# Kernel tuning notes

Hardware: AMD Instinct MI355X
Metric: run time of the kernel (lower is better)

Reference implementation:

```python
import jax, jax.numpy as jnp
import numpy as np

IN_F = 4096
OUT_F = 4096
N_VALS = 4096
N_TOKENS = 4096


def setup_inputs() -> dict:
    key = jax.random.key(0)
    k_x, k_v, k_i = jax.random.split(key, 3)
    x = jax.random.normal(k_x, (N_TOKENS, IN_F), dtype=jnp.float32)
    # codebook of memristor conductance differences (sorted, as in load_values)
    values = jnp.sort(jax.random.normal(k_v, (N_VALS,), dtype=jnp.float32))
    w_idx = jax.random.randint(k_i, (OUT_F, IN_F), 0, N_VALS, dtype=jnp.int64)
    bias = jnp.zeros((OUT_F,), dtype=jnp.float32)
    return {"x": x, "values": values, "w_idx": w_idx, "bias": bias}


def reference(x, values, w_idx, bias):
    # dequantize weight from codebook: (out_f, in_f)
    weight = values[w_idx]
    # F.linear(x, weight, bias) == x @ weight.T + bias
    return jnp.einsum("ti,oi->to", x, weight) + bias
```

## Files before the change

kernel.cpp:

```cpp
#include <hip/hip_runtime.h>
#include <hip/hip_bf16.h>
#include <stdint.h>

typedef unsigned short u16;
typedef __bf16 bf16x8 __attribute__((ext_vector_type(8)));
typedef float  f32x4  __attribute__((ext_vector_type(4)));
typedef u16    u16x8  __attribute__((ext_vector_type(8)));
typedef u16    u16x4  __attribute__((ext_vector_type(4)));

__device__ __forceinline__ u16 f2bf(float f) {
  union { float f; unsigned u; } v; v.f = f;
  unsigned u = v.u;
  unsigned r = u + 0x7FFFu + ((u >> 16) & 1u);
  return (u16)(r >> 16);
}

__device__ __forceinline__ void gld_lds16(const void* g, void* l) {
  __builtin_amdgcn_global_load_lds(
      (const __attribute__((address_space(1))) void*)g,
      (__attribute__((address_space(3))) void*)l, 16, 0, 0);
}

__global__ void detect_idx_width(const unsigned* __restrict__ w, int* __restrict__ flag) {
  unsigned v = w[threadIdx.x * 2 + 1];
  unsigned long long any = __ballot(v != 0u);
  if (threadIdx.x == 0) *flag = (any != 0ull) ? 1 : 0;
}

__global__ __launch_bounds__(256) void cvt_x_kernel(const float4* __restrict__ x,
                                                    u16* __restrict__ xb, long n8) {
  long i = (long)blockIdx.x * blockDim.x + threadIdx.x;
  long stride = (long)gridDim.x * blockDim.x;
  for (; i < n8; i += stride) {
    float4 a = x[2 * i];
    float4 b = x[2 * i + 1];
    u16x8 r;
    r[0] = f2bf(a.x); r[1] = f2bf(a.y); r[2] = f2bf(a.z); r[3] = f2bf(a.w);
    r[4] = f2bf(b.x); r[5] = f2bf(b.y); r[6] = f2bf(b.z); r[7] = f2bf(b.w);
    *(u16x8*)(xb + 8 * i) = r;
  }
}

__global__ __launch_bounds__(256) void dequant_w_kernel(const int4* __restrict__ widx,
                                                        const float* __restrict__ values,
                                                        u16* __restrict__ wb,
                                                        const int* __restrict__ flag, long n4) {
  const bool is32 = (*flag != 0);
  long i = (long)blockIdx.x * blockDim.x + threadIdx.x;
  long stride = (long)gridDim.x * blockDim.x;
  for (; i < n4; i += stride) {
    int i0, i1, i2, i3;
    if (is32) {
      int4 v = widx[i];
      i0 = v.x; i1 = v.y; i2 = v.z; i3 = v.w;
    } else {
      int4 a = widx[2 * i];
      int4 b = widx[2 * i + 1];
      i0 = a.x; i1 = a.z; i2 = b.x; i3 = b.z;
    }
    u16x4 r;
    r[0] = f2bf(values[i0]); r[1] = f2bf(values[i1]);
    r[2] = f2bf(values[i2]); r[3] = f2bf(values[i3]);
    *(u16x4*)(wb + 4 * i) = r;
  }
}

#define VMW(n) asm volatile("s_waitcnt vmcnt(" #n ")" ::: "memory")
#define PH_BAR asm volatile("s_barrier" ::: "memory")

__global__ __launch_bounds__(512, 1) void gemm256_kernel(
    const u16* __restrict__ Xb, const u16* __restrict__ Wb,
    const float* __restrict__ bias, float* __restrict__ C,
    int Nout, int Kin) {
  __shared__ __align__(16) char lds[163840];

  const int tid  = threadIdx.x;
  const int lane = tid & 63;
  const int wave = tid >> 6;
  const int wr = wave >> 2;
  const int wc = wave & 3;

  const int nwg = gridDim.x;
  const int bid = blockIdx.x;
  const int q8 = nwg >> 3, r8 = nwg & 7;
  const int xcd = bid & 7;
  const int wg = (xcd < r8 ? xcd * (q8 + 1) : r8 * (q8 + 1) + (xcd - r8) * q8) + (bid >> 3);

  const int tiles_n = Nout / 256;
  const long brow = (long)(wg / tiles_n) * 256;
  const long bcol = (long)(wg % tiles_n) * 256;

  const long rowb = (long)Kin * 2;
  const long rstep = 64 * rowb;
  const long hstep = 128 * rowb;

  const int f0  = tid * 16;
  const int f1  = f0 + 8192;
  const int rS0 = f0 >> 7;
  const int cS  = (f0 & 127) ^ ((rS0 & 7) << 4);
  const int voff = (int)(rS0 * rowb) + cS;

  const char* uA = (const char*)Xb + (size_t)brow * rowb;
  const char* uB = (const char*)Wb + (size_t)bcol * rowb;

#define STAGE_AH(base_, h, t) { \
  gld_lds16(uA + (size_t)(h) * hstep + (size_t)(t) * 128 + voff,         lds + (base_) + (h) * 16384 + f0); \
  gld_lds16(uA + (size_t)(h) * hstep + (size_t)(t) * 128 + rstep + voff, lds + (base_) + (h) * 16384 + f1); }
#define STAGE_BH(base_, h, t) { \
  gld_lds16(uB + (size_t)(h) * hstep + (size_t)(t) * 128 + voff,         lds + (base_) + (h) * 16384 + f0); \
  gld_lds16(uB + (size_t)(h) * hstep + (size_t)(t) * 128 + rstep + voff, lds + (base_) + (h) * 16384 + f1); }

  const int fr   = lane & 15;
  const int kb   = (lane >> 4) * 16;
  const int xsw  = (fr & 7) << 4;
  const int colx0 = kb ^ xsw;
  const int colx1 = (64 + kb) ^ xsw;
  const int aOff = wr * 16384 + fr * 128;
  const int bOff = (wc >> 1) * 16384 + ((wc & 1) * 64 + fr) * 128;

  bf16x8 afrA[2][2];
  bf16x8 afrB[2][2];
  bf16x8 bfrE[4][2];
  bf16x8 bfrO[4][2];
  f32x4  acc[8][4] = {};

#define READ_AQ(abase_, q, DST) { \
  const char* ab = lds + (abase_) + aOff + (q) * 4096; \
  DST[0][0] = *(const bf16x8*)(ab + colx0); \
  DST[0][1] = *(const bf16x8*)(ab + colx1); \
  DST[1][0] = *(const bf16x8*)(ab + 2048 + colx0); \
  DST[1][1] = *(const bf16x8*)(ab + 2048 + colx1); }

#define READ_BPF(bbase_, dst, lo) { \
  const char* bb = lds + (bbase_) + bOff; \
  dst[(lo)][0]     = *(const bf16x8*)(bb + (lo) * 2048 + colx0); \
  dst[(lo)][1]     = *(const bf16x8*)(bb + (lo) * 2048 + colx1); \
  dst[(lo) + 1][0] = *(const bf16x8*)(bb + ((lo) + 1) * 2048 + colx0); \
  dst[(lo) + 1][1] = *(const bf16x8*)(bb + ((lo) + 1) * 2048 + colx1); }

#define MFMA_Q(q, AF, BF) { \
  __builtin_amdgcn_s_setprio(1); \
  _Pragma("unroll") for (int m2 = 0; m2 < 2; ++m2) \
  _Pragma("unroll") for (int ni = 0; ni < 4; ++ni) { \
    acc[(q)*2+m2][ni] = __builtin_amdgcn_mfma_f32_16x16x32_bf16(AF[m2][0], BF[ni][0], acc[(q)*2+m2][ni], 0, 0, 0); \
    acc[(q)*2+m2][ni] = __builtin_amdgcn_mfma_f32_16x16x32_bf16(AF[m2][1], BF[ni][1], acc[(q)*2+m2][ni], 0, 0, 0); } \
  __builtin_amdgcn_s_setprio(0); }

#define PHASE(RDS, STG, MF, WT) { \
  RDS; STG; PH_BAR; MF; WT; PH_BAR; }

  const int aB0 = 0, aB1 = 32768;
  int bR0 = 65536, bR1 = 98304, bR2 = 131072;
  const int NT = Kin >> 6;

  STAGE_AH(aB0, 0, 0); STAGE_AH(aB0, 1, 0);
  STAGE_BH(bR0, 0, 0); STAGE_BH(bR0, 1, 0);
  if (NT > 1) { STAGE_BH(bR1, 0, 1); STAGE_BH(bR1, 1, 1); }
  if (NT > 2) { STAGE_BH(bR2, 0, 2); STAGE_BH(bR2, 1, 2); }
  VMW(0);
  PH_BAR;
  READ_BPF(bR0, bfrE, 0); READ_BPF(bR0, bfrE, 2);

  const int NITER = NT >> 1;
  for (int i = 0; i < NITER; ++i) {
    const int t0 = i * 2;
    const bool a1 = (t0 + 1 < NT);
    const bool a2 = (t0 + 2 < NT);
    const bool b3 = (t0 + 3 < NT);
    const bool b4 = (t0 + 4 < NT);

    PHASE({ READ_AQ(aB0, 0, afrA); READ_AQ(aB0, 1, afrB); },
          { if (a1) STAGE_AH(aB1, 0, t0 + 1); },
          MFMA_Q(0, afrA, bfrE), (void)0);
    PHASE({ READ_AQ(aB0, 2, afrA); if (a1) READ_BPF(bR1, bfrO, 0); },
          { if (a1) STAGE_AH(aB1, 1, t0 + 1); },
          MFMA_Q(1, afrB, bfrE), (void)0);
    PHASE({ READ_AQ(aB0, 3, afrB); if (a1) READ_BPF(bR1, bfrO, 2); },
          { if (b3) STAGE_BH(bR0, 0, t0 + 3); },
          MFMA_Q(2, afrA, bfrE), (void)0);
    PHASE({ (void)0; },
          { if (b3) STAGE_BH(bR0, 1, t0 + 3); },
          MFMA_Q(3, afrB, bfrE),
          { if (b3) { VMW(4); } else { VMW(0); } });

    PHASE({ READ_AQ(aB1, 0, afrA); READ_AQ(aB1, 1, afrB); },
          { if (a2) STAGE_AH(aB0, 0, t0 + 2); },
          MFMA_Q(0, afrA, bfrO), (void)0);
    PHASE({ READ_AQ(aB1, 2, afrA); if (a2) READ_BPF(bR2, bfrE, 0); },
          { if (a2) STAGE_AH(aB0, 1, t0 + 2); },
          MFMA_Q(1, afrB, bfrO), (void)0);
    PHASE({ READ_AQ(aB1, 3, afrB); if (a2) READ_BPF(bR2, bfrE, 2); },
          { if (b4) STAGE_BH(bR1, 0, t0 + 4); },
          MFMA_Q(2, afrA, bfrO), (void)0);
    PHASE({ (void)0; },
          { if (b4) STAGE_BH(bR1, 1, t0 + 4); },
          MFMA_Q(3, afrB, bfrO),
          { if (b4) { VMW(4); } else { VMW(0); } });

    int tmp = bR0; bR0 = bR2; bR2 = bR1; bR1 = tmp;
  }

  const int cm = (lane >> 4) * 4;
  const int cn = lane & 15;
  float bv[4];
#pragma unroll
  for (int ni = 0; ni < 4; ++ni) bv[ni] = bias[bcol + wc * 64 + ni * 16 + cn];

#pragma unroll
  for (int mi = 0; mi < 8; ++mi) {
    const long row0 = brow + wr * 128 + mi * 16 + cm;
#pragma unroll
    for (int ni = 0; ni < 4; ++ni) {
      const long col = bcol + wc * 64 + ni * 16 + cn;
#pragma unroll
      for (int j = 0; j < 4; ++j)
        C[(row0 + j) * (long)Nout + col] = acc[mi][ni][j] + bv[ni];
    }
  }
#undef STAGE_AH
#undef STAGE_BH
#undef READ_AQ
#undef READ_BPF
#undef MFMA_Q
#undef PHASE
}

__global__ __launch_bounds__(256, 2) void gemm128_kernel(
    const u16* __restrict__ Xb, const u16* __restrict__ Wb,
    const float* __restrict__ bias, float* __restrict__ C,
    int Nout, int Kin) {
  __shared__ __align__(16) u16 As[128 * 32];
  __shared__ __align__(16) u16 Bs[128 * 32];
  const int tid  = threadIdx.x;
  const int lane = tid & 63;
  const int wave = tid >> 6;
  const int wr = wave >> 1, wc = wave & 1;
  const int nwg = gridDim.x, bid = blockIdx.x;
  const int q = nwg >> 3, r8 = nwg & 7;
  const int xcd = bid & 7;
  const int wg = (xcd < r8 ? xcd * (q + 1) : r8 * (q + 1) + (xcd - r8) * q) + (bid >> 3);
  const int tiles_n = Nout / 128;
  const long brow = (long)(wg / tiles_n) * 128;
  const long bcol = (long)(wg % tiles_n) * 128;
  const int f0 = tid * 16, f1 = f0 + 4096;
  const size_t rowbytes = (size_t)Kin * 2;
  const char* gA0 = (const char*)Xb + (size_t)(brow + (f0 >> 6)) * rowbytes + (f0 & 63);
  const char* gA1 = (const char*)Xb + (size_t)(brow + (f1 >> 6)) * rowbytes + (f1 & 63);
  const char* gB0 = (const char*)Wb + (size_t)(bcol + (f0 >> 6)) * rowbytes + (f0 & 63);
  const char* gB1 = (const char*)Wb + (size_t)(bcol + (f1 >> 6)) * rowbytes + (f1 & 63);
  char* lA0 = (char*)As + f0; char* lA1 = (char*)As + f1;
  char* lB0 = (char*)Bs + f0; char* lB1 = (char*)Bs + f1;
  const int fr = lane & 15, kb = (lane >> 4) * 16;
  const char* aptr[4]; const char* bptr[4];
#pragma unroll
  for (int i = 0; i < 4; ++i) {
    aptr[i] = (const char*)As + (wr * 64 + i * 16 + fr) * 64 + kb;
    bptr[i] = (const char*)Bs + (wc * 64 + i * 16 + fr) * 64 + kb;
  }
  f32x4 acc[4][4] = {};
  for (int kk = 0; kk < Kin; kk += 32) {
    const size_t ko = (size_t)kk * 2;
    gld_lds16(gA0 + ko, lA0); gld_lds16(gA1 + ko, lA1);
    gld_lds16(gB0 + ko, lB0); gld_lds16(gB1 + ko, lB1);
    __syncthreads();
    bf16x8 a[4], b[4];
#pragma unroll
    for (int i = 0; i < 4; ++i) a[i] = *(const bf16x8*)aptr[i];
#pragma unroll
    for (int i = 0; i < 4; ++i) b[i] = *(const bf16x8*)bptr[i];
#pragma unroll
    for (int mi = 0; mi < 4; ++mi)
#pragma unroll
      for (int ni = 0; ni < 4; ++ni)
        acc[mi][ni] = __builtin_amdgcn_mfma_f32_16x16x32_bf16(a[mi], b[ni], acc[mi][ni], 0, 0, 0);
    __syncthreads();
  }
  const int cm = (lane >> 4) * 4, cn = lane & 15;
  float bv[4];
#pragma unroll
  for (int ni = 0; ni < 4; ++ni) bv[ni] = bias[bcol + wc * 64 + ni * 16 + cn];
#pragma unroll
  for (int mi = 0; mi < 4; ++mi) {
    const long row0 = brow + wr * 64 + mi * 16 + cm;
#pragma unroll
    for (int ni = 0; ni < 4; ++ni) {
      const long col = bcol + wc * 64 + ni * 16 + cn;
#pragma unroll
      for (int j = 0; j < 4; ++j)
        C[(row0 + j) * (long)Nout + col] = acc[mi][ni][j] + bv[ni];
    }
  }
}

__global__ void fallback_kernel(const float* __restrict__ x, const float* __restrict__ values,
                                const int* __restrict__ widx, const float* __restrict__ bias,
                                float* __restrict__ out, const int* __restrict__ flag,
                                int NT, int IF, int OF) {
  const int o = blockIdx.x * blockDim.x + threadIdx.x;
  const int t = blockIdx.y;
  if (o >= OF || t >= NT) return;
  const bool is32 = (*flag != 0);
  const float* xr = x + (size_t)t * IF;
  float sum = 0.f;
  if (is32) {
    const int* w = widx + (size_t)o * IF;
    for (int k = 0; k < IF; ++k) sum += xr[k] * values[w[k]];
  } else {
    const long long* w = (const long long*)widx + (size_t)o * IF;
    for (int k = 0; k < IF; ++k) sum += xr[k] * values[(int)w[k]];
  }
  out[(size_t)t * OF + o] = sum + bias[o];
}

extern "C" void kernel_launch(void* const* d_in, const int* in_sizes, int n_in,
                              void* d_out, int out_size, void* d_ws, size_t ws_size,
                              hipStream_t stream) {
  const float* x      = (const float*)d_in[0];
  const float* values = (const float*)d_in[1];
  const int*   widx   = (const int*)d_in[2];
  const float* bias   = (const float*)d_in[3];
  float* out = (float*)d_out;

  const long xsz = in_sizes[0];
  const int  OF  = in_sizes[3];
  const long wsz = in_sizes[2];
  const int  IF  = (int)(wsz / OF);
  const int  NTOK = (int)(xsz / IF);

  u16* xb = (u16*)d_ws;
  u16* wb = xb + (size_t)NTOK * IF;
  int* flag = (int*)(wb + (size_t)OF * IF);
  const size_t need = ((size_t)NTOK * IF + (size_t)OF * IF) * sizeof(u16) + 64;

  const bool pre_ok = (ws_size >= need) && ((xsz % 8) == 0) && ((wsz % 4) == 0);
  const bool f256 = pre_ok && (IF % 128 == 0) && (IF >= 256) &&
                    (NTOK % 256 == 0) && (OF % 256 == 0);
  const bool f128 = pre_ok && (IF % 32 == 0) && (NTOK % 128 == 0) && (OF % 128 == 0);

  if (f256 || f128) {
    hipLaunchKernelGGL(detect_idx_width, dim3(1), dim3(64), 0, stream,
                       (const unsigned*)widx, flag);
    hipLaunchKernelGGL(cvt_x_kernel, dim3(2048), dim3(256), 0, stream,
                       (const float4*)x, xb, xsz / 8);
    hipLaunchKernelGGL(dequant_w_kernel, dim3(2048), dim3(256), 0, stream,
                       (const int4*)widx, values, wb, (const int*)flag, wsz / 4);
    if (f256) {
      const int grid = (NTOK / 256) * (OF / 256);
      hipLaunchKernelGGL(gemm256_kernel, dim3(grid), dim3(512), 0, stream,
                         xb, wb, bias, out, OF, IF);
    } else {
      const int grid = (NTOK / 128) * (OF / 128);
      hipLaunchKernelGGL(gemm128_kernel, dim3(grid), dim3(256), 0, stream,
                         xb, wb, bias, out, OF, IF);
    }
  } else {
    int* flag2 = (int*)d_ws;
    hipLaunchKernelGGL(detect_idx_width, dim3(1), dim3(64), 0, stream,
                       (const unsigned*)widx, flag2);
    hipLaunchKernelGGL(fallback_kernel, dim3((OF + 255) / 256, NTOK), dim3(256), 0, stream,
                       x, values, widx, bias, out, (const int*)flag2, NTOK, IF, OF);
  }
}
```

Before: 170.8 us.

## Interleave LDS reads and global loads with MFMAs via sched_group_barrier; fuse prepass kernels

Rewrites the gemm256 main loop so that each phase interleaves individual MFMA pairs with single LDS fragment reads and global-to-LDS loads, using sched_group_barrier to pin the order. It also drops one barrier per phase, prefetches the next A fragment a phase ahead, and peels the last two iterations so the steady-state loop has no bounds checks. The x conversion and weight dequant kernels are merged into one launch. The aim is to hide LDS and global latency under matrix math and save a launch. The trade-off is fewer barriers with tighter wait counts, which raises the risk of LDS races, plus more register pressure from prefetched fragments.

After: 154.6 us. 9.5% less time.

```diff
diff --git a/kernel.cpp b/kernel.cpp
--- a/kernel.cpp
+++ b/kernel.cpp
@@ -27,11 +27,13 @@
   if (threadIdx.x == 0) *flag = (any != 0ull) ? 1 : 0;
 }
 
-__global__ __launch_bounds__(256) void cvt_x_kernel(const float4* __restrict__ x,
-                                                    u16* __restrict__ xb, long n8) {
-  long i = (long)blockIdx.x * blockDim.x + threadIdx.x;
-  long stride = (long)gridDim.x * blockDim.x;
-  for (; i < n8; i += stride) {
+__global__ __launch_bounds__(256) void prepass_kernel(
+    const float4* __restrict__ x, u16* __restrict__ xb, long n8,
+    const int4* __restrict__ widx, const float* __restrict__ values,
+    u16* __restrict__ wb, const int* __restrict__ flag, long n4) {
+  const long gid = (long)blockIdx.x * blockDim.x + threadIdx.x;
+  const long stride = (long)gridDim.x * blockDim.x;
+  for (long i = gid; i < n8; i += stride) {
     float4 a = x[2 * i];
     float4 b = x[2 * i + 1];
     u16x8 r;
@@ -39,16 +41,8 @@
     r[4] = f2bf(b.x); r[5] = f2bf(b.y); r[6] = f2bf(b.z); r[7] = f2bf(b.w);
     *(u16x8*)(xb + 8 * i) = r;
   }
-}
-
-__global__ __launch_bounds__(256) void dequant_w_kernel(const int4* __restrict__ widx,
-                                                        const float* __restrict__ values,
-                                                        u16* __restrict__ wb,
-                                                        const int* __restrict__ flag, long n4) {
   const bool is32 = (*flag != 0);
-  long i = (long)blockIdx.x * blockDim.x + threadIdx.x;
-  long stride = (long)gridDim.x * blockDim.x;
-  for (; i < n4; i += stride) {
+  for (long i = gid; i < n4; i += stride) {
     int i0, i1, i2, i3;
     if (is32) {
       int4 v = widx[i];
@@ -67,6 +61,8 @@
 
 #define VMW(n) asm volatile("s_waitcnt vmcnt(" #n ")" ::: "memory")
 #define PH_BAR asm volatile("s_barrier" ::: "memory")
+#define SGB(m, n) __builtin_amdgcn_sched_group_barrier((m), (n), 0)
+#define NOWT (void)0
 
 __global__ __launch_bounds__(512, 1) void gemm256_kernel(
     const u16* __restrict__ Xb, const u16* __restrict__ Wb,
@@ -90,7 +86,7 @@
   const long brow = (long)(wg / tiles_n) * 256;
   const long bcol = (long)(wg % tiles_n) * 256;
 
-  const long rowb = (long)Kin * 2;
+  const long rowb  = (long)Kin * 2;
   const long rstep = 64 * rowb;
   const long hstep = 128 * rowb;
 
@@ -103,12 +99,12 @@
   const char* uA = (const char*)Xb + (size_t)brow * rowb;
   const char* uB = (const char*)Wb + (size_t)bcol * rowb;
 
-#define STAGE_AH(base_, h, t) { \
-  gld_lds16(uA + (size_t)(h) * hstep + (size_t)(t) * 128 + voff,         lds + (base_) + (h) * 16384 + f0); \
-  gld_lds16(uA + (size_t)(h) * hstep + (size_t)(t) * 128 + rstep + voff, lds + (base_) + (h) * 16384 + f1); }
-#define STAGE_BH(base_, h, t) { \
-  gld_lds16(uB + (size_t)(h) * hstep + (size_t)(t) * 128 + voff,         lds + (base_) + (h) * 16384 + f0); \
-  gld_lds16(uB + (size_t)(h) * hstep + (size_t)(t) * 128 + rstep + voff, lds + (base_) + (h) * 16384 + f1); }
+#define SA1(base_, h, t, part) \
+  gld_lds16(uA + (size_t)(h) * hstep + (size_t)(t) * 128 + ((part) ? rstep : 0) + voff, \
+            lds + (base_) + (h) * 16384 + ((part) ? f1 : f0));
+#define SB1(base_, h, t, part) \
+  gld_lds16(uB + (size_t)(h) * hstep + (size_t)(t) * 128 + ((part) ? rstep : 0) + voff, \
+            lds + (base_) + (h) * 16384 + ((part) ? f1 : f0));
 
   const int fr   = lane & 15;
   const int kb   = (lane >> 4) * 16;
@@ -124,79 +120,118 @@
   bf16x8 bfrO[4][2];
   f32x4  acc[8][4] = {};
 
-#define READ_AQ(abase_, q, DST) { \
-  const char* ab = lds + (abase_) + aOff + (q) * 4096; \
-  DST[0][0] = *(const bf16x8*)(ab + colx0); \
-  DST[0][1] = *(const bf16x8*)(ab + colx1); \
-  DST[1][0] = *(const bf16x8*)(ab + 2048 + colx0); \
-  DST[1][1] = *(const bf16x8*)(ab + 2048 + colx1); }
-
-#define READ_BPF(bbase_, dst, lo) { \
-  const char* bb = lds + (bbase_) + bOff; \
-  dst[(lo)][0]     = *(const bf16x8*)(bb + (lo) * 2048 + colx0); \
-  dst[(lo)][1]     = *(const bf16x8*)(bb + (lo) * 2048 + colx1); \
-  dst[(lo) + 1][0] = *(const bf16x8*)(bb + ((lo) + 1) * 2048 + colx0); \
-  dst[(lo) + 1][1] = *(const bf16x8*)(bb + ((lo) + 1) * 2048 + colx1); }
-
-#define MFMA_Q(q, AF, BF) { \
-  __builtin_amdgcn_s_setprio(1); \
-  _Pragma("unroll") for (int m2 = 0; m2 < 2; ++m2) \
-  _Pragma("unroll") for (int ni = 0; ni < 4; ++ni) { \
-    acc[(q)*2+m2][ni] = __builtin_amdgcn_mfma_f32_16x16x32_bf16(AF[m2][0], BF[ni][0], acc[(q)*2+m2][ni], 0, 0, 0); \
-    acc[(q)*2+m2][ni] = __builtin_amdgcn_mfma_f32_16x16x32_bf16(AF[m2][1], BF[ni][1], acc[(q)*2+m2][ni], 0, 0, 0); } \
-  __builtin_amdgcn_s_setprio(0); }
-
-#define PHASE(RDS, STG, MF, WT) { \
-  RDS; STG; PH_BAR; MF; WT; PH_BAR; }
+#define RDA(abase_, q, DST, m2, ks) \
+  DST[(m2)][(ks)] = *(const bf16x8*)(lds + (abase_) + aOff + (q) * 4096 + (m2) * 2048 + ((ks) ? colx1 : colx0));
+#define RDB(bbase_, DST, ni, ks) \
+  DST[(ni)][(ks)] = *(const bf16x8*)(lds + (bbase_) + bOff + (ni) * 2048 + ((ks) ? colx1 : colx0));
+
+#define MFMA1(d, a, b) d = __builtin_amdgcn_mfma_f32_16x16x32_bf16((a), (b), (d), 0, 0, 0)
+#define MM2(q, m2, ni, AF, BF) { \
+  MFMA1(acc[(q)*2+(m2)][(ni)], AF[(m2)][0], BF[(ni)][0]); \
+  MFMA1(acc[(q)*2+(m2)][(ni)], AF[(m2)][1], BF[(ni)][1]); }
+
+#define PHASE(q, AF, BF, R0, R1, R2, R3, R4, R5, S0, S1, WT) { \
+  MM2(q, 0, 0, AF, BF); SGB(0x8, 2); R0; SGB(0x100, 1); \
+  MM2(q, 1, 0, AF, BF); SGB(0x8, 2); R1; SGB(0x100, 1); \
+  MM2(q, 0, 1, AF, BF); SGB(0x8, 2); R2; SGB(0x100, 1); \
+  MM2(q, 1, 1, AF, BF); SGB(0x8, 2); R3; SGB(0x100, 1); \
+  MM2(q, 0, 2, AF, BF); SGB(0x8, 2); R4; SGB(0x100, 1); \
+  MM2(q, 1, 2, AF, BF); SGB(0x8, 2); R5; SGB(0x100, 1); \
+  MM2(q, 0, 3, AF, BF); SGB(0x8, 2); S0; SGB(0x70, 1); \
+  MM2(q, 1, 3, AF, BF); SGB(0x8, 2); S1; SGB(0x70, 1); \
+  WT; PH_BAR; }
 
   const int aB0 = 0, aB1 = 32768;
   int bR0 = 65536, bR1 = 98304, bR2 = 131072;
   const int NT = Kin >> 6;
 
-  STAGE_AH(aB0, 0, 0); STAGE_AH(aB0, 1, 0);
-  STAGE_BH(bR0, 0, 0); STAGE_BH(bR0, 1, 0);
-  if (NT > 1) { STAGE_BH(bR1, 0, 1); STAGE_BH(bR1, 1, 1); }
-  if (NT > 2) { STAGE_BH(bR2, 0, 2); STAGE_BH(bR2, 1, 2); }
+  SA1(aB0, 0, 0, 0); SA1(aB0, 0, 0, 1); SA1(aB0, 1, 0, 0); SA1(aB0, 1, 0, 1);
+  SB1(bR0, 0, 0, 0); SB1(bR0, 0, 0, 1); SB1(bR0, 1, 0, 0); SB1(bR0, 1, 0, 1);
+  SB1(bR1, 0, 1, 0); SB1(bR1, 0, 1, 1); SB1(bR1, 1, 1, 0); SB1(bR1, 1, 1, 1);
+  SB1(bR2, 0, 2, 0); SB1(bR2, 0, 2, 1); SB1(bR2, 1, 2, 0); SB1(bR2, 1, 2, 1);
   VMW(0);
   PH_BAR;
-  READ_BPF(bR0, bfrE, 0); READ_BPF(bR0, bfrE, 2);
+  RDB(bR0, bfrE, 0, 0); RDB(bR0, bfrE, 0, 1); RDB(bR0, bfrE, 1, 0); RDB(bR0, bfrE, 1, 1);
+  RDB(bR0, bfrE, 2, 0); RDB(bR0, bfrE, 2, 1); RDB(bR0, bfrE, 3, 0); RDB(bR0, bfrE, 3, 1);
+  RDA(aB0, 0, afrA, 0, 0); RDA(aB0, 0, afrA, 0, 1); RDA(aB0, 0, afrA, 1, 0); RDA(aB0, 0, afrA, 1, 1);
 
   const int NITER = NT >> 1;
-  for (int i = 0; i < NITER; ++i) {
+  const int MAIN = NITER - 2;
+  for (int i = 0; i < MAIN; ++i) {
+    const int t0 = i * 2;
+    PHASE(0, afrA, bfrE,
+          RDA(aB0, 1, afrB, 0, 0), RDA(aB0, 1, afrB, 0, 1), RDA(aB0, 1, afrB, 1, 0), RDA(aB0, 1, afrB, 1, 1),
+          RDB(bR1, bfrO, 0, 0), RDB(bR1, bfrO, 0, 1),
+          SA1(aB1, 0, t0 + 1, 0), SA1(aB1, 0, t0 + 1, 1), NOWT);
+    PHASE(1, afrB, bfrE,
+          RDA(aB0, 2, afrA, 0, 0), RDA(aB0, 2, afrA, 0, 1), RDA(aB0, 2, afrA, 1, 0), RDA(aB0, 2, afrA, 1, 1),
+          RDB(bR1, bfrO, 1, 0), RDB(bR1, bfrO, 1, 1),
+          SA1(aB1, 1, t0 + 1, 0), SA1(aB1, 1, t0 + 1, 1), NOWT);
+    PHASE(2, afrA, bfrE,
+          RDA(aB0, 3, afrB, 0, 0), RDA(aB0, 3, afrB, 0, 1), RDA(aB0, 3, afrB, 1, 0), RDA(aB0, 3, afrB, 1, 1),
+          RDB(bR1, bfrO, 2, 0), RDB(bR1, bfrO, 2, 1),
+          SB1(bR0, 0, t0 + 3, 0), SB1(bR0, 0, t0 + 3, 1), VMW(2));
+    PHASE(3, afrB, bfrE,
+          RDA(aB1, 0, afrA, 0, 0), RDA(aB1, 0, afrA, 0, 1), RDA(aB1, 0, afrA, 1, 0), RDA(aB1, 0, afrA, 1, 1),
+          RDB(bR1, bfrO, 3, 0), RDB(bR1, bfrO, 3, 1),
+          SB1(bR0, 1, t0 + 3, 0), SB1(bR0, 1, t0 + 3, 1), NOWT);
+    PHASE(0, afrA, bfrO,
+          RDA(aB1, 1, afrB, 0, 0), RDA(aB1, 1, afrB, 0, 1), RDA(aB1, 1, afrB, 1, 0), RDA(aB1, 1, afrB, 1, 1),
+          RDB(bR2, bfrE, 0, 0), RDB(bR2, bfrE, 0, 1),
+          SA1(aB0, 0, t0 + 2, 0), SA1(aB0, 0, t0 + 2, 1), NOWT);
+    PHASE(1, afrB, bfrO,
+          RDA(aB1, 2, afrA, 0, 0), RDA(aB1, 2, afrA, 0, 1), RDA(aB1, 2, afrA, 1, 0), RDA(aB1, 2, afrA, 1, 1),
+          RDB(bR2, bfrE, 1, 0), RDB(bR2, bfrE, 1, 1),
+          SA1(aB0, 1, t0 + 2, 0), SA1(aB0, 1, t0 + 2, 1), NOWT);
+    PHASE(2, afrA, bfrO,
+          RDA(aB1, 3, afrB, 0, 0), RDA(aB1, 3, afrB, 0, 1), RDA(aB1, 3, afrB, 1, 0), RDA(aB1, 3, afrB, 1, 1),
+          RDB(bR2, bfrE, 2, 0), RDB(bR2, bfrE, 2, 1),
+          SB1(bR1, 0, t0 + 4, 0), SB1(bR1, 0, t0 + 4, 1), VMW(2));
+    PHASE(3, afrB, bfrO,
+          RDA(aB0, 0, afrA, 0, 0), RDA(aB0, 0, afrA, 0, 1), RDA(aB0, 0, afrA, 1, 0), RDA(aB0, 0, afrA, 1, 1),
+          RDB(bR2, bfrE, 3, 0), RDB(bR2, bfrE, 3, 1),
+          SB1(bR1, 1, t0 + 4, 0), SB1(bR1, 1, t0 + 4, 1), NOWT);
+    int tmp = bR0; bR0 = bR2; bR2 = bR1; bR1 = tmp;
+  }
+
+  for (int i = (MAIN > 0 ? MAIN : 0); i < NITER; ++i) {
     const int t0 = i * 2;
     const bool a1 = (t0 + 1 < NT);
     const bool a2 = (t0 + 2 < NT);
     const bool b3 = (t0 + 3 < NT);
     const bool b4 = (t0 + 4 < NT);
-
-    PHASE({ READ_AQ(aB0, 0, afrA); READ_AQ(aB0, 1, afrB); },
-          { if (a1) STAGE_AH(aB1, 0, t0 + 1); },
-          MFMA_Q(0, afrA, bfrE), (void)0);
-    PHASE({ READ_AQ(aB0, 2, afrA); if (a1) READ_BPF(bR1, bfrO, 0); },
-          { if (a1) STAGE_AH(aB1, 1, t0 + 1); },
-          MFMA_Q(1, afrB, bfrE), (void)0);
-    PHASE({ READ_AQ(aB0, 3, afrB); if (a1) READ_BPF(bR1, bfrO, 2); },
-          { if (b3) STAGE_BH(bR0, 0, t0 + 3); },
-          MFMA_Q(2, afrA, bfrE), (void)0);
-    PHASE({ (void)0; },
-          { if (b3) STAGE_BH(bR0, 1, t0 + 3); },
-          MFMA_Q(3, afrB, bfrE),
-          { if (b3) { VMW(4); } else { VMW(0); } });
-
-    PHASE({ READ_AQ(aB1, 0, afrA); READ_AQ(aB1, 1, afrB); },
-          { if (a2) STAGE_AH(aB0, 0, t0 + 2); },
-          MFMA_Q(0, afrA, bfrO), (void)0);
-    PHASE({ READ_AQ(aB1, 2, afrA); if (a2) READ_BPF(bR2, bfrE, 0); },
-          { if (a2) STAGE_AH(aB0, 1, t0 + 2); },
-          MFMA_Q(1, afrB, bfrO), (void)0);
-    PHASE({ READ_AQ(aB1, 3, afrB); if (a2) READ_BPF(bR2, bfrE, 2); },
-          { if (b4) STAGE_BH(bR1, 0, t0 + 4); },
-          MFMA_Q(2, afrA, bfrO), (void)0);
-    PHASE({ (void)0; },
-          { if (b4) STAGE_BH(bR1, 1, t0 + 4); },
-          MFMA_Q(3, afrB, bfrO),
-          { if (b4) { VMW(4); } else { VMW(0); } });
-
+    PHASE(0, afrA, bfrE,
+          RDA(aB0, 1, afrB, 0, 0), RDA(aB0, 1, afrB, 0, 1), RDA(aB0, 1, afrB, 1, 0), RDA(aB0, 1, afrB, 1, 1),
+          RDB(bR1, bfrO, 0, 0), RDB(bR1, bfrO, 0, 1),
+          { if (a1) SA1(aB1, 0, t0 + 1, 0) }, { if (a1) SA1(aB1, 0, t0 + 1, 1) }, NOWT);
+    PHASE(1, afrB, bfrE,
+          RDA(aB0, 2, afrA, 0, 0), RDA(aB0, 2, afrA, 0, 1), RDA(aB0, 2, afrA, 1, 0), RDA(aB0, 2, afrA, 1, 1),
+          RDB(bR1, bfrO, 1, 0), RDB(bR1, bfrO, 1, 1),
+          { if (a1) SA1(aB1, 1, t0 + 1, 0) }, { if (a1) SA1(aB1, 1, t0 + 1, 1) }, NOWT);
+    PHASE(2, afrA, bfrE,
+          RDA(aB0, 3, afrB, 0, 0), RDA(aB0, 3, afrB, 0, 1), RDA(aB0, 3, afrB, 1, 0), RDA(aB0, 3, afrB, 1, 1),
+          RDB(bR1, bfrO, 2, 0), RDB(bR1, bfrO, 2, 1),
+          { if (b3) SB1(bR0, 0, t0 + 3, 0) }, { if (b3) SB1(bR0, 0, t0 + 3, 1) }, VMW(0));
+    PHASE(3, afrB, bfrE,
+          RDA(aB1, 0, afrA, 0, 0), RDA(aB1, 0, afrA, 0, 1), RDA(aB1, 0, afrA, 1, 0), RDA(aB1, 0, afrA, 1, 1),
+          RDB(bR1, bfrO, 3, 0), RDB(bR1, bfrO, 3, 1),
+          { if (b3) SB1(bR0, 1, t0 + 3, 0) }, { if (b3) SB1(bR0, 1, t0 + 3, 1) }, NOWT);
+    PHASE(0, afrA, bfrO,
+          RDA(aB1, 1, afrB, 0, 0), RDA(aB1, 1, afrB, 0, 1), RDA(aB1, 1, afrB, 1, 0), RDA(aB1, 1, afrB, 1, 1),
+          RDB(bR2, bfrE, 0, 0), RDB(bR2, bfrE, 0, 1),
+          { if (a2) SA1(aB0, 0, t0 + 2, 0) }, { if (a2) SA1(aB0, 0, t0 + 2, 1) }, NOWT);
+    PHASE(1, afrB, bfrO,
+          RDA(aB1, 2, afrA, 0, 0), RDA(aB1, 2, afrA, 0, 1), RDA(aB1, 2, afrA, 1, 0), RDA(aB1, 2, afrA, 1, 1),
+          RDB(bR2, bfrE, 1, 0), RDB(bR2, bfrE, 1, 1),
+          { if (a2) SA1(aB0, 1, t0 + 2, 0) }, { if (a2) SA1(aB0, 1, t0 + 2, 1) }, NOWT);
+    PHASE(2, afrA, bfrO,
+          RDA(aB1, 3, afrB, 0, 0), RDA(aB1, 3, afrB, 0, 1), RDA(aB1, 3, afrB, 1, 0), RDA(aB1, 3, afrB, 1, 1),
+          RDB(bR2, bfrE, 2, 0), RDB(bR2, bfrE, 2, 1),
+          { if (b4) SB1(bR1, 0, t0 + 4, 0) }, { if (b4) SB1(bR1, 0, t0 + 4, 1) }, VMW(0));
+    PHASE(3, afrB, bfrO,
+          RDA(aB0, 0, afrA, 0, 0), RDA(aB0, 0, afrA, 0, 1), RDA(aB0, 0, afrA, 1, 0), RDA(aB0, 0, afrA, 1, 1),
+          RDB(bR2, bfrE, 3, 0), RDB(bR2, bfrE, 3, 1),
+          { if (b4) SB1(bR1, 1, t0 + 4, 0) }, { if (b4) SB1(bR1, 1, t0 + 4, 1) }, NOWT);
     int tmp = bR0; bR0 = bR2; bR2 = bR1; bR1 = tmp;
   }
 
@@ -217,11 +252,12 @@
         C[(row0 + j) * (long)Nout + col] = acc[mi][ni][j] + bv[ni];
     }
   }
-#undef STAGE_AH
-#undef STAGE_BH
-#undef READ_AQ
-#undef READ_BPF
-#undef MFMA_Q
+#undef SA1
+#undef SB1
+#undef RDA
+#undef RDB
+#undef MFMA1
+#undef MM2
 #undef PHASE
 }
 
@@ -340,9 +376,8 @@
   if (f256 || f128) {
     hipLaunchKernelGGL(detect_idx_width, dim3(1), dim3(64), 0, stream,
                        (const unsigned*)widx, flag);
-    hipLaunchKernelGGL(cvt_x_kernel, dim3(2048), dim3(256), 0, stream,
-                       (const float4*)x, xb, xsz / 8);
-    hipLaunchKernelGGL(dequant_w_kernel, dim3(2048), dim3(256), 0, stream,
+    hipLaunchKernelGGL(prepass_kernel, dim3(2048), dim3(256), 0, stream,
+                       (const float4*)x, xb, xsz / 8,
                        (const int4*)widx, values, wb, (const int*)flag, wsz / 4);
     if (f256) {
       const int grid = (NTOK / 256) * (OF / 256);
```

## Load B fragments directly from global into registers and interleave via sched_group_barrier

Applied to the files above, without the earlier changes.

The B (weight) tile no longer passes through LDS. Each wave loads its B fragments straight from global memory into registers, one k-tile ahead, which cuts LDS from 160KB to 64KB and drops the triple-buffered B ring. The per-phase barriers are replaced by sched_group_barrier hints that interleave each MFMA pair with one LDS read or one global load, and the loop keeps only one barrier pair per k-tile. In exchange, wc-pairs now load the same B rows redundantly from global/L2, the B reads are less coalesced, and global latency has to be hidden inside a single tile's worth of MFMAs.

New measurement: 232.2 us. 36.0% more time.

```diff
diff --git a/kernel.cpp b/kernel.cpp
--- a/kernel.cpp
+++ b/kernel.cpp
@@ -67,12 +67,13 @@
 
 #define VMW(n) asm volatile("s_waitcnt vmcnt(" #n ")" ::: "memory")
 #define PH_BAR asm volatile("s_barrier" ::: "memory")
+#define SGB(m, n) __builtin_amdgcn_sched_group_barrier((m), (n), 0)
 
 __global__ __launch_bounds__(512, 1) void gemm256_kernel(
     const u16* __restrict__ Xb, const u16* __restrict__ Wb,
     const float* __restrict__ bias, float* __restrict__ C,
     int Nout, int Kin) {
-  __shared__ __align__(16) char lds[163840];
+  __shared__ __align__(16) char lds[65536];
 
   const int tid  = threadIdx.x;
   const int lane = tid & 63;
@@ -90,7 +91,7 @@
   const long brow = (long)(wg / tiles_n) * 256;
   const long bcol = (long)(wg % tiles_n) * 256;
 
-  const long rowb = (long)Kin * 2;
+  const long rowb  = (long)Kin * 2;
   const long rstep = 64 * rowb;
   const long hstep = 128 * rowb;
 
@@ -103,12 +104,9 @@
   const char* uA = (const char*)Xb + (size_t)brow * rowb;
   const char* uB = (const char*)Wb + (size_t)bcol * rowb;
 
-#define STAGE_AH(base_, h, t) { \
-  gld_lds16(uA + (size_t)(h) * hstep + (size_t)(t) * 128 + voff,         lds + (base_) + (h) * 16384 + f0); \
-  gld_lds16(uA + (size_t)(h) * hstep + (size_t)(t) * 128 + rstep + voff, lds + (base_) + (h) * 16384 + f1); }
-#define STAGE_BH(base_, h, t) { \
-  gld_lds16(uB + (size_t)(h) * hstep + (size_t)(t) * 128 + voff,         lds + (base_) + (h) * 16384 + f0); \
-  gld_lds16(uB + (size_t)(h) * hstep + (size_t)(t) * 128 + rstep + voff, lds + (base_) + (h) * 16384 + f1); }
+#define SA1(base_, h, t, part) \
+  gld_lds16(uA + (size_t)(h) * hstep + (size_t)(t) * 128 + ((part) ? rstep : 0) + voff, \
+            lds + (base_) + (h) * 16384 + ((part) ? f1 : f0))
 
   const int fr   = lane & 15;
   const int kb   = (lane >> 4) * 16;
@@ -116,7 +114,10 @@
   const int colx0 = kb ^ xsw;
   const int colx1 = (64 + kb) ^ xsw;
   const int aOff = wr * 16384 + fr * 128;
-  const int bOff = (wc >> 1) * 16384 + ((wc & 1) * 64 + fr) * 128;
+  const int aAdr0 = aOff + colx0;
+  const int aAdr1 = aOff + colx1;
+
+  const int voffB = (int)((wc * 64 + fr) * rowb) + kb;
 
   bf16x8 afrA[2][2];
   bf16x8 afrB[2][2];
@@ -124,80 +125,116 @@
   bf16x8 bfrO[4][2];
   f32x4  acc[8][4] = {};
 
-#define READ_AQ(abase_, q, DST) { \
-  const char* ab = lds + (abase_) + aOff + (q) * 4096; \
-  DST[0][0] = *(const bf16x8*)(ab + colx0); \
-  DST[0][1] = *(const bf16x8*)(ab + colx1); \
-  DST[1][0] = *(const bf16x8*)(ab + 2048 + colx0); \
-  DST[1][1] = *(const bf16x8*)(ab + 2048 + colx1); }
-
-#define READ_BPF(bbase_, dst, lo) { \
-  const char* bb = lds + (bbase_) + bOff; \
-  dst[(lo)][0]     = *(const bf16x8*)(bb + (lo) * 2048 + colx0); \
-  dst[(lo)][1]     = *(const bf16x8*)(bb + (lo) * 2048 + colx1); \
-  dst[(lo) + 1][0] = *(const bf16x8*)(bb + ((lo) + 1) * 2048 + colx0); \
-  dst[(lo) + 1][1] = *(const bf16x8*)(bb + ((lo) + 1) * 2048 + colx1); }
-
-#define MFMA_Q(q, AF, BF) { \
-  __builtin_amdgcn_s_setprio(1); \
-  _Pragma("unroll") for (int m2 = 0; m2 < 2; ++m2) \
-  _Pragma("unroll") for (int ni = 0; ni < 4; ++ni) { \
-    acc[(q)*2+m2][ni] = __builtin_amdgcn_mfma_f32_16x16x32_bf16(AF[m2][0], BF[ni][0], acc[(q)*2+m2][ni], 0, 0, 0); \
-    acc[(q)*2+m2][ni] = __builtin_amdgcn_mfma_f32_16x16x32_bf16(AF[m2][1], BF[ni][1], acc[(q)*2+m2][ni], 0, 0, 0); } \
-  __builtin_amdgcn_s_setprio(0); }
-
-#define PHASE(RDS, STG, MF, WT) { \
-  RDS; STG; PH_BAR; MF; WT; PH_BAR; }
+#define RDA(aBase_, q, DST, m2, ks) \
+  DST[(m2)][(ks)] = *(const bf16x8*)(lds + ((ks) ? aAdr1 : aAdr0) + (aBase_) + (q) * 4096 + (m2) * 2048)
+#define LDB(DST, ni, ks, tt) \
+  DST[(ni)][(ks)] = *(const bf16x8*)(uB + (size_t)(ni) * 16 * rowb + (size_t)(tt) * 128 + (ks) * 64 + voffB)
+
+#define MFMA1(d, a, b) d = __builtin_amdgcn_mfma_f32_16x16x32_bf16((a), (b), (d), 0, 0, 0)
+#define MM2(q, m2, ni, AF, BF) { \
+  MFMA1(acc[(q)*2+(m2)][(ni)], AF[(m2)][0], BF[(ni)][0]); \
+  MFMA1(acc[(q)*2+(m2)][(ni)], AF[(m2)][1], BF[(ni)][1]); }
+
+#define DSLOT(x) x; SGB(0x100, 1)
+#define VSLOT(x) x; SGB(0x70, 1)
+
+#define PHASE(q, AF, BF, S1, S2, S3, S4, S5, S6, S7, S8) { \
+  MM2(q, 0, 0, AF, BF); SGB(0x8, 2); S1; \
+  MM2(q, 1, 0, AF, BF); SGB(0x8, 2); S2; \
+  MM2(q, 0, 1, AF, BF); SGB(0x8, 2); S3; \
+  MM2(q, 1, 1, AF, BF); SGB(0x8, 2); S4; \
+  MM2(q, 0, 2, AF, BF); SGB(0x8, 2); S5; \
+  MM2(q, 1, 2, AF, BF); SGB(0x8, 2); S6; \
+  MM2(q, 0, 3, AF, BF); SGB(0x8, 2); S7; \
+  MM2(q, 1, 3, AF, BF); SGB(0x8, 2); S8; }
+
+#define MFMA_PH(q, AF, BF) { \
+  MM2(q, 0, 0, AF, BF); MM2(q, 1, 0, AF, BF); MM2(q, 0, 1, AF, BF); MM2(q, 1, 1, AF, BF); \
+  MM2(q, 0, 2, AF, BF); MM2(q, 1, 2, AF, BF); MM2(q, 0, 3, AF, BF); MM2(q, 1, 3, AF, BF); }
 
   const int aB0 = 0, aB1 = 32768;
-  int bR0 = 65536, bR1 = 98304, bR2 = 131072;
   const int NT = Kin >> 6;
 
-  STAGE_AH(aB0, 0, 0); STAGE_AH(aB0, 1, 0);
-  STAGE_BH(bR0, 0, 0); STAGE_BH(bR0, 1, 0);
-  if (NT > 1) { STAGE_BH(bR1, 0, 1); STAGE_BH(bR1, 1, 1); }
-  if (NT > 2) { STAGE_BH(bR2, 0, 2); STAGE_BH(bR2, 1, 2); }
+  SA1(aB0, 0, 0, 0); SA1(aB0, 0, 0, 1); SA1(aB0, 1, 0, 0); SA1(aB0, 1, 0, 1);
+  LDB(bfrE, 0, 0, 0); LDB(bfrE, 0, 1, 0); LDB(bfrE, 1, 0, 0); LDB(bfrE, 1, 1, 0);
+  LDB(bfrE, 2, 0, 0); LDB(bfrE, 2, 1, 0); LDB(bfrE, 3, 0, 0); LDB(bfrE, 3, 1, 0);
   VMW(0);
   PH_BAR;
-  READ_BPF(bR0, bfrE, 0); READ_BPF(bR0, bfrE, 2);
+  RDA(aB0, 0, afrA, 0, 0); RDA(aB0, 0, afrA, 0, 1);
+  RDA(aB0, 0, afrA, 1, 0); RDA(aB0, 0, afrA, 1, 1);
 
   const int NITER = NT >> 1;
   for (int i = 0; i < NITER; ++i) {
     const int t0 = i * 2;
-    const bool a1 = (t0 + 1 < NT);
-    const bool a2 = (t0 + 2 < NT);
-    const bool b3 = (t0 + 3 < NT);
-    const bool b4 = (t0 + 4 < NT);
-
-    PHASE({ READ_AQ(aB0, 0, afrA); READ_AQ(aB0, 1, afrB); },
-          { if (a1) STAGE_AH(aB1, 0, t0 + 1); },
-          MFMA_Q(0, afrA, bfrE), (void)0);
-    PHASE({ READ_AQ(aB0, 2, afrA); if (a1) READ_BPF(bR1, bfrO, 0); },
-          { if (a1) STAGE_AH(aB1, 1, t0 + 1); },
-          MFMA_Q(1, afrB, bfrE), (void)0);
-    PHASE({ READ_AQ(aB0, 3, afrB); if (a1) READ_BPF(bR1, bfrO, 2); },
-          { if (b3) STAGE_BH(bR0, 0, t0 + 3); },
-          MFMA_Q(2, afrA, bfrE), (void)0);
-    PHASE({ (void)0; },
-          { if (b3) STAGE_BH(bR0, 1, t0 + 3); },
-          MFMA_Q(3, afrB, bfrE),
-          { if (b3) { VMW(4); } else { VMW(0); } });
-
-    PHASE({ READ_AQ(aB1, 0, afrA); READ_AQ(aB1, 1, afrB); },
-          { if (a2) STAGE_AH(aB0, 0, t0 + 2); },
-          MFMA_Q(0, afrA, bfrO), (void)0);
-    PHASE({ READ_AQ(aB1, 2, afrA); if (a2) READ_BPF(bR2, bfrE, 0); },
-          { if (a2) STAGE_AH(aB0, 1, t0 + 2); },
-          MFMA_Q(1, afrB, bfrO), (void)0);
-    PHASE({ READ_AQ(aB1, 3, afrB); if (a2) READ_BPF(bR2, bfrE, 2); },
-          { if (b4) STAGE_BH(bR1, 0, t0 + 4); },
-          MFMA_Q(2, afrA, bfrO), (void)0);
-    PHASE({ (void)0; },
-          { if (b4) STAGE_BH(bR1, 1, t0 + 4); },
-          MFMA_Q(3, afrB, bfrO),
-          { if (b4) { VMW(4); } else { VMW(0); } });
-
-    int tmp = bR0; bR0 = bR2; bR2 = bR1; bR1 = tmp;
+    const int tn = (t0 + 2 < NT) ? t0 + 2 : t0;
+
+    PHASE(0, afrA, bfrE,
+          DSLOT(RDA(aB0, 1, afrB, 0, 0)),
+          DSLOT(RDA(aB0, 1, afrB, 0, 1)),
+          DSLOT(RDA(aB0, 1, afrB, 1, 0)),
+          DSLOT(RDA(aB0, 1, afrB, 1, 1)),
+          VSLOT(SA1(aB1, 0, t0 + 1, 0)),
+          VSLOT(SA1(aB1, 0, t0 + 1, 1)),
+          VSLOT(LDB(bfrO, 0, 0, t0 + 1)),
+          VSLOT(LDB(bfrO, 0, 1, t0 + 1)))
+    PHASE(1, afrB, bfrE,
+          DSLOT(RDA(aB0, 2, afrA, 0, 0)),
+          DSLOT(RDA(aB0, 2, afrA, 0, 1)),
+          DSLOT(RDA(aB0, 2, afrA, 1, 0)),
+          DSLOT(RDA(aB0, 2, afrA, 1, 1)),
+          VSLOT(SA1(aB1, 1, t0 + 1, 0)),
+          VSLOT(SA1(aB1, 1, t0 + 1, 1)),
+          VSLOT(LDB(bfrO, 1, 0, t0 + 1)),
+          VSLOT(LDB(bfrO, 1, 1, t0 + 1)))
+    PHASE(2, afrA, bfrE,
+          DSLOT(RDA(aB0, 3, afrB, 0, 0)),
+          DSLOT(RDA(aB0, 3, afrB, 0, 1)),
+          DSLOT(RDA(aB0, 3, afrB, 1, 0)),
+          DSLOT(RDA(aB0, 3, afrB, 1, 1)),
+          VSLOT(LDB(bfrO, 2, 0, t0 + 1)),
+          VSLOT(LDB(bfrO, 2, 1, t0 + 1)),
+          VSLOT(LDB(bfrO, 3, 0, t0 + 1)),
+          VSLOT(LDB(bfrO, 3, 1, t0 + 1)))
+    MFMA_PH(3, afrB, bfrE)
+    VMW(0);
+    PH_BAR;
+    RDA(aB1, 0, afrA, 0, 0); RDA(aB1, 0, afrA, 0, 1);
+    RDA(aB1, 0, afrA, 1, 0); RDA(aB1, 0, afrA, 1, 1);
+    PH_BAR;
+
+    PHASE(0, afrA, bfrO,
+          DSLOT(RDA(aB1, 1, afrB, 0, 0)),
+          DSLOT(RDA(aB1, 1, afrB, 0, 1)),
+          DSLOT(RDA(aB1, 1, afrB, 1, 0)),
+          DSLOT(RDA(aB1, 1, afrB, 1, 1)),
+          VSLOT(SA1(aB0, 0, tn, 0)),
+          VSLOT(SA1(aB0, 0, tn, 1)),
+          VSLOT(LDB(bfrE, 0, 0, tn)),
+          VSLOT(LDB(bfrE, 0, 1, tn)))
+    PHASE(1, afrB, bfrO,
+          DSLOT(RDA(aB1, 2, afrA, 0, 0)),
+          DSLOT(RDA(aB1, 2, afrA, 0, 1)),
+          DSLOT(RDA(aB1, 2, afrA, 1, 0)),
+          DSLOT(RDA(aB1, 2, afrA, 1, 1)),
+          VSLOT(SA1(aB0, 1, tn, 0)),
+          VSLOT(SA1(aB0, 1, tn, 1)),
+          VSLOT(LDB(bfrE, 1, 0, tn)),
+          VSLOT(LDB(bfrE, 1, 1, tn)))
+    PHASE(2, afrA, bfrO,
+          DSLOT(RDA(aB1, 3, afrB, 0, 0)),
+          DSLOT(RDA(aB1, 3, afrB, 0, 1)),
+          DSLOT(RDA(aB1, 3, afrB, 1, 0)),
+          DSLOT(RDA(aB1, 3, afrB, 1, 1)),
+          VSLOT(LDB(bfrE, 2, 0, tn)),
+          VSLOT(LDB(bfrE, 2, 1, tn)),
+          VSLOT(LDB(bfrE, 3, 0, tn)),
+          VSLOT(LDB(bfrE, 3, 1, tn)))
+    MFMA_PH(3, afrB, bfrO)
+    VMW(0);
+    PH_BAR;
+    RDA(aB0, 0, afrA, 0, 0); RDA(aB0, 0, afrA, 0, 1);
+    RDA(aB0, 0, afrA, 1, 0); RDA(aB0, 0, afrA, 1, 1);
+    PH_BAR;
   }
 
   const int cm = (lane >> 4) * 4;
@@ -217,12 +254,15 @@
         C[(row0 + j) * (long)Nout + col] = acc[mi][ni][j] + bv[ni];
     }
   }
-#undef STAGE_AH
-#undef STAGE_BH
-#undef READ_AQ
-#undef READ_BPF
-#undef MFMA_Q
+#undef SA1
+#undef RDA
+#undef LDB
+#undef MFMA1
+#undef MM2
+#undef DSLOT
+#undef VSLOT
 #undef PHASE
+#undef MFMA_PH
 }
 
 __global__ __launch_bounds__(256, 2) void gemm128_kernel(
```
